# Optimization experiments

Hardware: AMD Instinct MI355X
Metric: run time of the kernel (lower is better)

The kernel has to match this reference:

```python
import jax, jax.numpy as jnp
import numpy as np

B, N, H, L = 4096, 512, 1024, 8


def setup_inputs() -> dict:
    key = jax.random.key(0)
    k1, k2, k3, k4 = jax.random.split(key, 4)
    x = jax.random.normal(k1, (B, N), dtype=jnp.float32)
    beta = jax.random.uniform(k2, (H, L, N), dtype=jnp.float32)  # torch.rand init
    bound = 1.0 / np.sqrt(N)
    W = jax.random.uniform(k3, (H, N), minval=-bound, maxval=bound, dtype=jnp.float32)
    b = jax.random.uniform(k4, (H,), minval=-bound, maxval=bound, dtype=jnp.float32)
    return {"x": x, "beta": beta, "W": W, "b": b}


def reference(x, beta, W, b):
    # Original computes c[h,j,k] = sum_l beta[h,l,j]*beta[h,l,k], then
    # out_fm[b,h] = sum_{j<k} x[b,j]*x[b,k]*c[h,j,k]  (strict upper-tri mask).
    # FM identity: sum_{j<k} x_j x_k <v_j, v_k>
    #            = 0.5 * sum_l [ (sum_j x_j v_{lj})^2 - sum_j x_j^2 v_{lj}^2 ]
    s = jnp.einsum('bn,hln->bhl', x, beta)            # (B, H, L)
    ssq = jnp.einsum('bn,hln->bhl', x * x, beta * beta)  # (B, H, L)
    fm = 0.5 * jnp.sum(s * s - ssq, axis=-1)          # (B, H)
    linear_out = x @ W.T + b                          # (B, H)
    return fm + linear_out
```

## Files before the change

kernel.cpp:

```cpp
#include <hip/hip_runtime.h>
#include <stdint.h>

static constexpr int B_DIM = 4096;
static constexpr int N_DIM = 512;
static constexpr int H_DIM = 1024;
static constexpr int L_DIM = 8;
static constexpr int HL    = H_DIM * L_DIM;
static constexpr int KC    = 2 * N_DIM;

typedef __attribute__((ext_vector_type(8))) short short8;
typedef __attribute__((ext_vector_type(4))) float f32x4;

#define BK 32

__device__ __forceinline__ uint16_t f2bf(float f) {
  uint32_t u = __float_as_uint(f);
  u += 0x7fffu + ((u >> 16) & 1u);
  return (uint16_t)(u >> 16);
}

__device__ __forceinline__ void stage16(const uint16_t* g, uint16_t* l) {
  __builtin_amdgcn_global_load_lds(
      (const __attribute__((address_space(1))) void*)g,
      (__attribute__((address_space(3))) void*)l, 16, 0, 0);
}

__global__ void prep_kernel(const float* __restrict__ x, const float* __restrict__ beta,
                            const float* __restrict__ W,
                            uint16_t* __restrict__ xcomb, uint16_t* __restrict__ betab,
                            uint16_t* __restrict__ combW) {
  int idx = blockIdx.x * 256 + threadIdx.x;
  if (idx < HL * N_DIM) {
    betab[idx] = f2bf(beta[idx]);
    return;
  }
  idx -= HL * N_DIM;
  if (idx < B_DIM * N_DIM) {
    int b = idx >> 9, n = idx & 511;
    float v = x[idx];
    xcomb[(size_t)b * KC + n]         = f2bf(v);
    xcomb[(size_t)b * KC + N_DIM + n] = f2bf(v * v);
    return;
  }
  idx -= B_DIM * N_DIM;
  int h = idx >> 9, n = idx & 511;
  combW[(size_t)h * KC + n] = f2bf(W[idx]);
  float s = 0.f;
#pragma unroll
  for (int l = 0; l < L_DIM; ++l) {
    float v = beta[((size_t)h * L_DIM + l) * N_DIM + n];
    s += v * v;
  }
  combW[(size_t)h * KC + N_DIM + n] = f2bf(-0.5f * s);
}

template <int BM_, int BN_, int KTOT, bool FM>
__global__ __launch_bounds__(256) void gemm_kernel(
    const uint16_t* __restrict__ A,
    const uint16_t* __restrict__ Bt,
    const float* __restrict__ bias,
    float* __restrict__ out)
{
  constexpr int LDA = KC;
  constexpr int LDB = FM ? N_DIM : KC;
  constexpr int MI  = BM_ / 32;
  constexpr int NJ  = BN_ / 32;
  constexpr int CHA = BM_ * BK / 8;
  constexpr int CHB = BN_ * BK / 8;

  __shared__ __align__(16) uint16_t As[BM_ * BK];
  __shared__ __align__(16) uint16_t Bs[BN_ * BK];

  const int tid  = threadIdx.x;
  const int lane = tid & 63;
  const int wave = tid >> 6;
  const int wm = wave >> 1, wn = wave & 1;

  const int row0 = blockIdx.y * BM_;
  const int col0 = blockIdx.x * BN_;

  f32x4 acc[MI][NJ] = {};

  const int fr   = lane & 15;
  const int quad = lane >> 4;

  for (int kt = 0; kt < KTOT; kt += BK) {
#pragma unroll
    for (int s = tid; s < CHA; s += 256) {
      int m = s >> 2, cp = s & 3, c = cp ^ ((m >> 1) & 3);
      stage16(A + (size_t)(row0 + m) * LDA + kt + c * 8, As + s * 8);
    }
#pragma unroll
    for (int s = tid; s < CHB; s += 256) {
      int m = s >> 2, cp = s & 3, c = cp ^ ((m >> 1) & 3);
      stage16(Bt + (size_t)(col0 + m) * LDB + kt + c * 8, Bs + s * 8);
    }
    __syncthreads();

    short8 af[MI], bfr[NJ];
#pragma unroll
    for (int i = 0; i < MI; ++i) {
      int m = wm * (BM_ / 2) + i * 16 + fr;
      int cp = quad ^ ((m >> 1) & 3);
      af[i] = *(const short8*)(As + (m * 4 + cp) * 8);
    }
#pragma unroll
    for (int j = 0; j < NJ; ++j) {
      int m = wn * (BN_ / 2) + j * 16 + fr;
      int cp = quad ^ ((m >> 1) & 3);
      bfr[j] = *(const short8*)(Bs + (m * 4 + cp) * 8);
    }
#pragma unroll
    for (int i = 0; i < MI; ++i)
#pragma unroll
      for (int j = 0; j < NJ; ++j)
        acc[i][j] = __builtin_amdgcn_mfma_f32_16x16x32_bf16(af[i], bfr[j], acc[i][j], 0, 0, 0);
    __syncthreads();
  }

  if (FM) {
    const int hcol0 = blockIdx.x * (BN_ / L_DIM);
#pragma unroll
    for (int i = 0; i < MI; ++i) {
#pragma unroll
      for (int j = 0; j < NJ; ++j) {
        const int h_in = wn * (BN_ / 16) + j * 2 + (fr >> 3);
        const int rowb = row0 + wm * (BM_ / 2) + i * 16 + quad * 4;
#pragma unroll
        for (int r = 0; r < 4; ++r) {
          float v = acc[i][j][r];
          v = v * v;
          v += __shfl_xor(v, 1);
          v += __shfl_xor(v, 2);
          v += __shfl_xor(v, 4);
          if ((lane & 7) == 0)
            out[(size_t)(rowb + r) * H_DIM + hcol0 + h_in] = 0.5f * v;
        }
      }
    }
  } else {
#pragma unroll
    for (int i = 0; i < MI; ++i) {
#pragma unroll
      for (int j = 0; j < NJ; ++j) {
        const int col  = col0 + wn * (BN_ / 2) + j * 16 + fr;
        const int rowb = row0 + wm * (BM_ / 2) + i * 16 + quad * 4;
        const float bs = bias[col];
#pragma unroll
        for (int r = 0; r < 4; ++r) {
          size_t o = (size_t)(rowb + r) * H_DIM + col;
          out[o] += acc[i][j][r] + bs;
        }
      }
    }
  }
}

extern "C" void kernel_launch(void* const* d_in, const int* in_sizes, int n_in,
                              void* d_out, int out_size, void* d_ws, size_t ws_size,
                              hipStream_t stream) {
  const float* x    = (const float*)d_in[0];
  const float* beta = (const float*)d_in[1];
  const float* W    = (const float*)d_in[2];
  const float* bias = (const float*)d_in[3];
  float* out = (float*)d_out;

  uint16_t* xcomb = (uint16_t*)d_ws;
  uint16_t* betab = xcomb + (size_t)B_DIM * KC;
  uint16_t* combW = betab + (size_t)HL * N_DIM;

  const int prep_elems = HL * N_DIM + B_DIM * N_DIM + H_DIM * N_DIM;
  prep_kernel<<<(prep_elems + 255) / 256, 256, 0, stream>>>(x, beta, W, xcomb, betab, combW);

  gemm_kernel<128, 128, N_DIM, true><<<dim3(HL / 128, B_DIM / 128), 256, 0, stream>>>(
      xcomb, betab, nullptr, out);
  gemm_kernel<128, 64, KC, false><<<dim3(H_DIM / 64, B_DIM / 128), 256, 0, stream>>>(
      xcomb, combW, bias, out);
}
```

Baseline: 165.6 us.

## Fuse FM and linear GEMMs into one launch with atomic accumulation, BK=64

Merges the two GEMM launches into a single kernel whose grid is split by blockIdx.x between the FM tiles and the linear tiles. Both write into the output with atomicAdd, and the prep kernel now zeroes the output first. The K tile doubles to 64 with an 8-way XOR swizzle, halving the barrier count per tile. This removes a launch and the serialization between the two GEMMs, at the cost of atomic writes and more LDS per block.

```diff
diff --git a/kernel.cpp b/kernel.cpp
--- a/kernel.cpp
+++ b/kernel.cpp
@@ -11,7 +11,7 @@
 typedef __attribute__((ext_vector_type(8))) short short8;
 typedef __attribute__((ext_vector_type(4))) float f32x4;
 
-#define BK 32
+#define BK 64
 
 __device__ __forceinline__ uint16_t f2bf(float f) {
   uint32_t u = __float_as_uint(f);
@@ -28,7 +28,7 @@
 __global__ void prep_kernel(const float* __restrict__ x, const float* __restrict__ beta,
                             const float* __restrict__ W,
                             uint16_t* __restrict__ xcomb, uint16_t* __restrict__ betab,
-                            uint16_t* __restrict__ combW) {
+                            uint16_t* __restrict__ combW, float* __restrict__ out) {
   int idx = blockIdx.x * 256 + threadIdx.x;
   if (idx < HL * N_DIM) {
     betab[idx] = f2bf(beta[idx]);
@@ -43,89 +43,86 @@
     return;
   }
   idx -= B_DIM * N_DIM;
-  int h = idx >> 9, n = idx & 511;
-  combW[(size_t)h * KC + n] = f2bf(W[idx]);
-  float s = 0.f;
-#pragma unroll
-  for (int l = 0; l < L_DIM; ++l) {
-    float v = beta[((size_t)h * L_DIM + l) * N_DIM + n];
-    s += v * v;
-  }
-  combW[(size_t)h * KC + N_DIM + n] = f2bf(-0.5f * s);
-}
-
-template <int BM_, int BN_, int KTOT, bool FM>
-__global__ __launch_bounds__(256) void gemm_kernel(
-    const uint16_t* __restrict__ A,
-    const uint16_t* __restrict__ Bt,
+  if (idx < H_DIM * N_DIM) {
+    int h = idx >> 9, n = idx & 511;
+    combW[(size_t)h * KC + n] = f2bf(W[idx]);
+    float s = 0.f;
+#pragma unroll
+    for (int l = 0; l < L_DIM; ++l) {
+      float v = beta[((size_t)h * L_DIM + l) * N_DIM + n];
+      s += v * v;
+    }
+    combW[(size_t)h * KC + N_DIM + n] = f2bf(-0.5f * s);
+    return;
+  }
+  idx -= H_DIM * N_DIM;
+  f32x4 z = {0.f, 0.f, 0.f, 0.f};
+  ((f32x4*)out)[idx] = z;
+}
+
+__global__ __launch_bounds__(256) void fused_gemm_kernel(
+    const uint16_t* __restrict__ xcomb,
+    const uint16_t* __restrict__ betab,
+    const uint16_t* __restrict__ combW,
     const float* __restrict__ bias,
     float* __restrict__ out)
 {
-  constexpr int LDA = KC;
-  constexpr int LDB = FM ? N_DIM : KC;
-  constexpr int MI  = BM_ / 32;
-  constexpr int NJ  = BN_ / 32;
-  constexpr int CHA = BM_ * BK / 8;
-  constexpr int CHB = BN_ * BK / 8;
-
-  __shared__ __align__(16) uint16_t As[BM_ * BK];
-  __shared__ __align__(16) uint16_t Bs[BN_ * BK];
+  __shared__ __align__(16) uint16_t As[128 * BK];
+  __shared__ __align__(16) uint16_t Bs[128 * BK];
 
   const int tid  = threadIdx.x;
   const int lane = tid & 63;
   const int wave = tid >> 6;
   const int wm = wave >> 1, wn = wave & 1;
-
-  const int row0 = blockIdx.y * BM_;
-  const int col0 = blockIdx.x * BN_;
-
-  f32x4 acc[MI][NJ] = {};
-
   const int fr   = lane & 15;
   const int quad = lane >> 4;
-
-  for (int kt = 0; kt < KTOT; kt += BK) {
-#pragma unroll
-    for (int s = tid; s < CHA; s += 256) {
-      int m = s >> 2, cp = s & 3, c = cp ^ ((m >> 1) & 3);
-      stage16(A + (size_t)(row0 + m) * LDA + kt + c * 8, As + s * 8);
-    }
-#pragma unroll
-    for (int s = tid; s < CHB; s += 256) {
-      int m = s >> 2, cp = s & 3, c = cp ^ ((m >> 1) & 3);
-      stage16(Bt + (size_t)(col0 + m) * LDB + kt + c * 8, Bs + s * 8);
-    }
-    __syncthreads();
-
-    short8 af[MI], bfr[NJ];
-#pragma unroll
-    for (int i = 0; i < MI; ++i) {
-      int m = wm * (BM_ / 2) + i * 16 + fr;
-      int cp = quad ^ ((m >> 1) & 3);
-      af[i] = *(const short8*)(As + (m * 4 + cp) * 8);
-    }
-#pragma unroll
-    for (int j = 0; j < NJ; ++j) {
-      int m = wn * (BN_ / 2) + j * 16 + fr;
-      int cp = quad ^ ((m >> 1) & 3);
-      bfr[j] = *(const short8*)(Bs + (m * 4 + cp) * 8);
-    }
-#pragma unroll
-    for (int i = 0; i < MI; ++i)
-#pragma unroll
-      for (int j = 0; j < NJ; ++j)
-        acc[i][j] = __builtin_amdgcn_mfma_f32_16x16x32_bf16(af[i], bfr[j], acc[i][j], 0, 0, 0);
-    __syncthreads();
-  }
-
-  if (FM) {
-    const int hcol0 = blockIdx.x * (BN_ / L_DIM);
-#pragma unroll
-    for (int i = 0; i < MI; ++i) {
-#pragma unroll
-      for (int j = 0; j < NJ; ++j) {
-        const int h_in = wn * (BN_ / 16) + j * 2 + (fr >> 3);
-        const int rowb = row0 + wm * (BM_ / 2) + i * 16 + quad * 4;
+  const int row0 = blockIdx.y * 128;
+
+  if (blockIdx.x < 64) {
+    const int col0 = blockIdx.x * 128;
+    f32x4 acc[4][4] = {};
+    for (int kt = 0; kt < N_DIM; kt += BK) {
+#pragma unroll
+      for (int u = 0; u < 4; ++u) {
+        int s = tid + u * 256, m = s >> 3, cp = s & 7, c = cp ^ (m & 7);
+        stage16(xcomb + (size_t)(row0 + m) * KC + kt + c * 8, As + s * 8);
+      }
+#pragma unroll
+      for (int u = 0; u < 4; ++u) {
+        int s = tid + u * 256, m = s >> 3, cp = s & 7, c = cp ^ (m & 7);
+        stage16(betab + (size_t)(col0 + m) * N_DIM + kt + c * 8, Bs + s * 8);
+      }
+      __syncthreads();
+#pragma unroll
+      for (int kk = 0; kk < BK; kk += 32) {
+        short8 af[4], bf[4];
+#pragma unroll
+        for (int i = 0; i < 4; ++i) {
+          int m = wm * 64 + i * 16 + fr;
+          int cp = ((kk >> 3) + quad) ^ (m & 7);
+          af[i] = *(const short8*)(As + (m * 8 + cp) * 8);
+        }
+#pragma unroll
+        for (int j = 0; j < 4; ++j) {
+          int m = wn * 64 + j * 16 + fr;
+          int cp = ((kk >> 3) + quad) ^ (m & 7);
+          bf[j] = *(const short8*)(Bs + (m * 8 + cp) * 8);
+        }
+#pragma unroll
+        for (int i = 0; i < 4; ++i)
+#pragma unroll
+          for (int j = 0; j < 4; ++j)
+            acc[i][j] = __builtin_amdgcn_mfma_f32_16x16x32_bf16(af[i], bf[j], acc[i][j], 0, 0, 0);
+      }
+      __syncthreads();
+    }
+    const int hcol0 = blockIdx.x * 16;
+#pragma unroll
+    for (int i = 0; i < 4; ++i) {
+#pragma unroll
+      for (int j = 0; j < 4; ++j) {
+        const int h_in = wn * 8 + j * 2 + (fr >> 3);
+        const int rowb = row0 + wm * 64 + i * 16 + quad * 4;
 #pragma unroll
         for (int r = 0; r < 4; ++r) {
           float v = acc[i][j][r];
@@ -134,23 +131,58 @@
           v += __shfl_xor(v, 2);
           v += __shfl_xor(v, 4);
           if ((lane & 7) == 0)
-            out[(size_t)(rowb + r) * H_DIM + hcol0 + h_in] = 0.5f * v;
+            atomicAdd(out + (size_t)(rowb + r) * H_DIM + hcol0 + h_in, 0.5f * v);
         }
       }
     }
   } else {
-#pragma unroll
-    for (int i = 0; i < MI; ++i) {
-#pragma unroll
-      for (int j = 0; j < NJ; ++j) {
-        const int col  = col0 + wn * (BN_ / 2) + j * 16 + fr;
-        const int rowb = row0 + wm * (BM_ / 2) + i * 16 + quad * 4;
+    const int col0 = (blockIdx.x - 64) * 64;
+    f32x4 acc[4][2] = {};
+    for (int kt = 0; kt < KC; kt += BK) {
+#pragma unroll
+      for (int u = 0; u < 4; ++u) {
+        int s = tid + u * 256, m = s >> 3, cp = s & 7, c = cp ^ (m & 7);
+        stage16(xcomb + (size_t)(row0 + m) * KC + kt + c * 8, As + s * 8);
+      }
+#pragma unroll
+      for (int u = 0; u < 2; ++u) {
+        int s = tid + u * 256, m = s >> 3, cp = s & 7, c = cp ^ (m & 7);
+        stage16(combW + (size_t)(col0 + m) * KC + kt + c * 8, Bs + s * 8);
+      }
+      __syncthreads();
+#pragma unroll
+      for (int kk = 0; kk < BK; kk += 32) {
+        short8 af[4], bf[2];
+#pragma unroll
+        for (int i = 0; i < 4; ++i) {
+          int m = wm * 64 + i * 16 + fr;
+          int cp = ((kk >> 3) + quad) ^ (m & 7);
+          af[i] = *(const short8*)(As + (m * 8 + cp) * 8);
+        }
+#pragma unroll
+        for (int j = 0; j < 2; ++j) {
+          int m = wn * 32 + j * 16 + fr;
+          int cp = ((kk >> 3) + quad) ^ (m & 7);
+          bf[j] = *(const short8*)(Bs + (m * 8 + cp) * 8);
+        }
+#pragma unroll
+        for (int i = 0; i < 4; ++i)
+#pragma unroll
+          for (int j = 0; j < 2; ++j)
+            acc[i][j] = __builtin_amdgcn_mfma_f32_16x16x32_bf16(af[i], bf[j], acc[i][j], 0, 0, 0);
+      }
+      __syncthreads();
+    }
+#pragma unroll
+    for (int i = 0; i < 4; ++i) {
+#pragma unroll
+      for (int j = 0; j < 2; ++j) {
+        const int col  = col0 + wn * 32 + j * 16 + fr;
+        const int rowb = row0 + wm * 64 + i * 16 + quad * 4;
         const float bs = bias[col];
 #pragma unroll
-        for (int r = 0; r < 4; ++r) {
-          size_t o = (size_t)(rowb + r) * H_DIM + col;
-          out[o] += acc[i][j][r] + bs;
-        }
+        for (int r = 0; r < 4; ++r)
+          atomicAdd(out + (size_t)(rowb + r) * H_DIM + col, acc[i][j][r] + bs);
       }
     }
   }
@@ -169,11 +201,8 @@
   uint16_t* betab = xcomb + (size_t)B_DIM * KC;
   uint16_t* combW = betab + (size_t)HL * N_DIM;
 
-  const int prep_elems = HL * N_DIM + B_DIM * N_DIM + H_DIM * N_DIM;
-  prep_kernel<<<(prep_elems + 255) / 256, 256, 0, stream>>>(x, beta, W, xcomb, betab, combW);
-
-  gemm_kernel<128, 128, N_DIM, true><<<dim3(HL / 128, B_DIM / 128), 256, 0, stream>>>(
-      xcomb, betab, nullptr, out);
-  gemm_kernel<128, 64, KC, false><<<dim3(H_DIM / 64, B_DIM / 128), 256, 0, stream>>>(
-      xcomb, combW, bias, out);
-}
+  const int prep_elems = HL * N_DIM + B_DIM * N_DIM + H_DIM * N_DIM + B_DIM * H_DIM / 4;
+  prep_kernel<<<(prep_elems + 255) / 256, 256, 0, stream>>>(x, beta, W, xcomb, betab, combW, out);
+
+  fused_gemm_kernel<<<dim3(80, 32), 256, 0, stream>>>(xcomb, betab, combW, bias, out);
+}
```

After: 232.1 us. +40.1%, slower.
